# Kernel tuning notes

Hardware: AMD Instinct MI355X
Metric: run time of the kernel (lower is better)

## Reference

```python
import jax, jax.numpy as jnp
import numpy as np

B, S, D, H = 2, 2048, 1024, 16
DK = D // H

def setup_inputs() -> dict:
    key = jax.random.key(0)
    ks = jax.random.split(key, 10)
    s = 1.0 / np.sqrt(D)
    x = jax.random.normal(ks[0], (B, S, D), dtype=jnp.float32)
    # causal mask [B,1,S,S]: 1 = keep, 0 = masked
    mask = jnp.broadcast_to(jnp.tril(jnp.ones((S, S), dtype=jnp.int32))[None, None], (B, 1, S, S))
    wq = jax.random.uniform(ks[1], (D, D), jnp.float32, -s, s)
    bq = jax.random.uniform(ks[2], (D,), jnp.float32, -s, s)
    wk = jax.random.uniform(ks[3], (D, D), jnp.float32, -s, s)
    bk = jax.random.uniform(ks[4], (D,), jnp.float32, -s, s)
    wv = jax.random.uniform(ks[5], (D, D), jnp.float32, -s, s)
    bv = jax.random.uniform(ks[6], (D,), jnp.float32, -s, s)
    wo = jax.random.uniform(ks[7], (D, D), jnp.float32, -s, s)
    bo = jax.random.uniform(ks[8], (D,), jnp.float32, -s, s)
    return {"x": x, "mask": mask, "wq": wq, "bq": bq, "wk": wk, "bk": bk,
            "wv": wv, "bv": bv, "wo": wo, "bo": bo}

def reference(x, mask, wq, bq, wk, bk, wv, bv, wo, bo):
    # projections; torch Linear: y = x @ W^T + b
    def proj(w, b):
        return (jnp.einsum('bsd,ed->bse', x, w) + b).reshape(B, S, H, DK).transpose(0, 2, 1, 3)
    q = proj(wq, bq)  # [B,H,S,DK]
    k = proj(wk, bk)
    v = proj(wv, bv)
    scores = jnp.einsum('bhsd,bhtd->bhst', q, k) / np.sqrt(DK)  # [B,H,S,S]
    scores = jnp.where(mask == 0, jnp.float32(-1e9), scores)
    attn = jax.nn.softmax(scores, axis=-1)
    # dropout in eval mode -> identity
    out = jnp.einsum('bhst,bhtd->bhsd', attn, v)  # [B,H,S,DK]
    out = out.transpose(0, 2, 1, 3).reshape(B, S, D)
    return jnp.einsum('bsd,ed->bse', out, wo) + bo
```

## Files before the change

kernel.cpp:

```cpp
#include <hip/hip_runtime.h>
#include <hip/hip_bf16.h>

#define BB 2
#define SS 2048
#define DD 1024
#define HH 16
#define DK 64
#define MM (BB*SS)

typedef __attribute__((ext_vector_type(8))) short bf16x8;
typedef __attribute__((ext_vector_type(4))) float f32x4;

__device__ inline ushort f2bf(float f) {
  __hip_bfloat16 h = __float2bfloat16(f);
  return *reinterpret_cast<ushort*>(&h);
}

__device__ __forceinline__ float exp2_hw(float x) {
  float r; asm("v_exp_f32 %0, %1" : "=v"(r) : "v"(x)); return r;
}

__device__ __forceinline__ void gl_lds16(const ushort* g, ushort* l) {
  __builtin_amdgcn_global_load_lds((const __attribute__((address_space(1))) void*)g,
                                   (__attribute__((address_space(3))) void*)l, 16, 0, 0);
}

__global__ void cvt_f32_bf16(const float* __restrict__ src, ushort* __restrict__ dst, int n4) {
  int i = blockIdx.x * blockDim.x + threadIdx.x;
  int stride = gridDim.x * blockDim.x;
  for (int idx = i; idx < n4; idx += stride) {
    float4 v = reinterpret_cast<const float4*>(src)[idx];
    ushort4 o;
    o.x = f2bf(v.x); o.y = f2bf(v.y); o.z = f2bf(v.z); o.w = f2bf(v.w);
    reinterpret_cast<ushort4*>(dst)[idx] = o;
  }
}

__global__ void cvt3_f32_bf16(const float* __restrict__ s0, const float* __restrict__ s1,
                              const float* __restrict__ s2, ushort* __restrict__ dst) {
  const int n4seg = DD * DD / 4;
  int i = blockIdx.x * blockDim.x + threadIdx.x;
  int stride = gridDim.x * blockDim.x;
  for (int idx = i; idx < 3 * n4seg; idx += stride) {
    int seg = idx / n4seg;
    int off = idx - seg * n4seg;
    const float* s = (seg == 0) ? s0 : (seg == 1) ? s1 : s2;
    float4 v = reinterpret_cast<const float4*>(s)[off];
    ushort4 o;
    o.x = f2bf(v.x); o.y = f2bf(v.y); o.z = f2bf(v.z); o.w = f2bf(v.w);
    reinterpret_cast<ushort4*>(dst)[idx] = o;
  }
}

__global__ __launch_bounds__(256, 3) void gemm_qkv(const ushort* __restrict__ A,
                                                   const ushort* __restrict__ Wqkv,
                                                   const float* __restrict__ bq,
                                                   const float* __restrict__ bk,
                                                   const float* __restrict__ bv,
                                                   ushort* __restrict__ Qo,
                                                   ushort* __restrict__ Ko,
                                                   ushort* __restrict__ Vo,
                                                   float qscale) {
  constexpr int K = 1024;
  __shared__ __align__(16) ushort lA[128 * 64];
  __shared__ __align__(16) ushort lB[128 * 64];
  const int t = threadIdx.x;
  const int w = t >> 6, lane = t & 63;
  const int flat = blockIdx.x + 24 * blockIdx.y;
  const int xcd = flat & 7, idx = flat >> 3;
  const int m0 = ((xcd << 2) + (idx & 3)) * 128;
  const int n0 = (idx >> 2) * 128;
  const int wm = (w >> 1) * 64, wn = (w & 1) * 64;
  const int c = lane & 15, g = lane >> 4;

  f32x4 acc[4][4];
  #pragma unroll
  for (int i = 0; i < 4; i++)
    #pragma unroll
    for (int j = 0; j < 4; j++) acc[i][j] = f32x4{0.f, 0.f, 0.f, 0.f};

  auto stage = [&](int ks) {
    const int k0 = ks * 64;
    #pragma unroll
    for (int i = 0; i < 4; i++) {
      int ch = w * 256 + i * 64 + lane;
      int row = ch >> 3;
      int cs = (ch & 7) ^ (row & 7);
      gl_lds16(&A[(size_t)(m0 + row) * K + k0 + cs * 8], &lA[(w * 256 + i * 64) * 8]);
      gl_lds16(&Wqkv[(size_t)(n0 + row) * K + k0 + cs * 8], &lB[(w * 256 + i * 64) * 8]);
    }
  };

  for (int ks = 0; ks < 16; ks++) {
    stage(ks);
    __syncthreads();
    #pragma unroll
    for (int kk2 = 0; kk2 < 2; kk2++) {
      bf16x8 af[4], bfr[4];
      #pragma unroll
      for (int mi = 0; mi < 4; mi++) {
        int row = wm + mi * 16 + c;
        af[mi] = *reinterpret_cast<const bf16x8*>(&lA[row * 64 + (((kk2 * 4 + g) ^ (c & 7)) * 8)]);
      }
      #pragma unroll
      for (int ni = 0; ni < 4; ni++) {
        int row = wn + ni * 16 + c;
        bfr[ni] = *reinterpret_cast<const bf16x8*>(&lB[row * 64 + (((kk2 * 4 + g) ^ (c & 7)) * 8)]);
      }
      #pragma unroll
      for (int mi = 0; mi < 4; mi++)
        #pragma unroll
        for (int ni = 0; ni < 4; ni++)
          acc[mi][ni] = __builtin_amdgcn_mfma_f32_16x16x32_bf16(af[mi], bfr[ni], acc[mi][ni], 0, 0, 0);
    }
    __syncthreads();
  }

  const int seg = n0 >> 10;
  const float* bp = (seg == 0) ? bq : (seg == 1) ? bk : bv;
  ushort* op = (seg == 0) ? Qo : Ko;
  const float sc = (seg == 0) ? qscale : 1.0f;
  #pragma unroll
  for (int mi = 0; mi < 4; mi++) {
    #pragma unroll
    for (int ni = 0; ni < 4; ni++) {
      int colq = (n0 + wn + ni * 16 + c) & 1023;
      float bvv = bp[colq];
      int h = colq >> 6, dk = colq & 63;
      #pragma unroll
      for (int j = 0; j < 4; j++) {
        int row = m0 + wm + mi * 16 + g * 4 + j;
        int b = row >> 11, s = row & 2047;
        float val = (acc[mi][ni][j] + bvv) * sc;
        if (seg == 2) {
          Vo[(((b * HH + h) * DK + dk) << 11) + s] = f2bf(val);
        } else {
          op[(((b * HH + h) * SS + s) << 6) + dk] = f2bf(val);
        }
      }
    }
  }
}

__global__ __launch_bounds__(256, 2) void gemm_out(const ushort* __restrict__ A,
                                                   const ushort* __restrict__ W,
                                                   const float* __restrict__ bias,
                                                   float* __restrict__ out) {
  constexpr int K = 1024;
  __shared__ __align__(16) ushort lA[2][64 * 64];
  __shared__ __align__(16) ushort lB[2][128 * 64];
  const int t = threadIdx.x;
  const int w = t >> 6, lane = t & 63;
  const int flat = blockIdx.x + 8 * blockIdx.y;
  const int swz = (flat & 7) * 64 + (flat >> 3);
  const int m0 = (swz >> 3) * 64, n0 = (swz & 7) * 128;
  const int wm = (w >> 1) * 32, wn = (w & 1) * 64;
  const int c = lane & 15, g = lane >> 4;

  f32x4 acc[2][4];
  #pragma unroll
  for (int i = 0; i < 2; i++)
    #pragma unroll
    for (int j = 0; j < 4; j++) acc[i][j] = f32x4{0.f, 0.f, 0.f, 0.f};

  auto stage = [&](int ks, int buf) {
    const int k0 = ks * 64;
    #pragma unroll
    for (int i = 0; i < 2; i++) {
      int ch = i * 256 + t;
      int row = ch >> 3;
      int cs = (ch & 7) ^ (row & 7);
      gl_lds16(&A[(size_t)(m0 + row) * K + k0 + cs * 8], &lA[buf][(i * 256 + w * 64) * 8]);
    }
    #pragma unroll
    for (int i = 0; i < 4; i++) {
      int ch = i * 256 + t;
      int row = ch >> 3;
      int cs = (ch & 7) ^ (row & 7);
      gl_lds16(&W[(size_t)(n0 + row) * K + k0 + cs * 8], &lB[buf][(i * 256 + w * 64) * 8]);
    }
  };

  stage(0, 0);
  __syncthreads();
  int cur = 0;
  for (int ks = 0; ks < 16; ks++) {
    if (ks + 1 < 16) stage(ks + 1, cur ^ 1);
    #pragma unroll
    for (int kk2 = 0; kk2 < 2; kk2++) {
      bf16x8 af[2], bfr[4];
      #pragma unroll
      for (int mi = 0; mi < 2; mi++) {
        int row = wm + mi * 16 + c;
        af[mi] = *reinterpret_cast<const bf16x8*>(&lA[cur][row * 64 + (((kk2 * 4 + g) ^ (c & 7)) * 8)]);
      }
      #pragma unroll
      for (int ni = 0; ni < 4; ni++) {
        int row = wn + ni * 16 + c;
        bfr[ni] = *reinterpret_cast<const bf16x8*>(&lB[cur][row * 64 + (((kk2 * 4 + g) ^ (c & 7)) * 8)]);
      }
      #pragma unroll
      for (int mi = 0; mi < 2; mi++)
        #pragma unroll
        for (int ni = 0; ni < 4; ni++)
          acc[mi][ni] = __builtin_amdgcn_mfma_f32_16x16x32_bf16(af[mi], bfr[ni], acc[mi][ni], 0, 0, 0);
    }
    __syncthreads();
    cur ^= 1;
  }

  #pragma unroll
  for (int mi = 0; mi < 2; mi++) {
    #pragma unroll
    for (int ni = 0; ni < 4; ni++) {
      int colb = n0 + wn + ni * 16 + c;
      float bv = bias[colb];
      #pragma unroll
      for (int j = 0; j < 4; j++) {
        int row = m0 + wm + mi * 16 + g * 4 + j;
        out[(row << 10) + colb] = acc[mi][ni][j] + bv;
      }
    }
  }
}

__global__ __launch_bounds__(256, 2) void attn_fwd(const ushort* __restrict__ Q,
                                                   const ushort* __restrict__ Kk,
                                                   const ushort* __restrict__ Vt,
                                                   ushort* __restrict__ O) {
  __shared__ __align__(16) ushort ldsK[2][64 * 64];
  __shared__ __align__(16) ushort ldsV[2][64 * 64];
  __shared__ __align__(16) ushort lds_p[4][16 * 72];
  const int t0 = threadIdx.x;
  const int w = t0 >> 6;
  const int lane = t0 & 63;
  const int c = lane & 15, g = lane >> 4;
  const int flat = blockIdx.x + 16 * blockIdx.y;
  const int swz = (flat & 7) * 64 + (flat >> 3);
  const int bx = swz & 15;
  const int bh = swz >> 4;
  const int a = bx * 4 + w;
  const int rb0 = a * 16;
  const int rb1 = 2032 - a * 16;
  const int itB = (2111 - 16 * a) >> 6;
  const int itMax = (2111 - 64 * bx) >> 6;

  const ushort* qbase = Q + (size_t)bh * SS * DK;
  const ushort* kbase = Kk + (size_t)bh * SS * DK;
  const ushort* vbase = Vt + (size_t)bh * DK * SS;

  bf16x8 onesf;
  #pragma unroll
  for (int i = 0; i < 8; i++) onesf[i] = (short)0x3F80;

  bf16x8 qf[2][2];
  qf[0][0] = *reinterpret_cast<const bf16x8*>(&qbase[(rb0 + c) * DK + g * 8]);
  qf[0][1] = *reinterpret_cast<const bf16x8*>(&qbase[(rb0 + c) * DK + 32 + g * 8]);
  qf[1][0] = *reinterpret_cast<const bf16x8*>(&qbase[(rb1 + c) * DK + g * 8]);
  qf[1][1] = *reinterpret_cast<const bf16x8*>(&qbase[(rb1 + c) * DK + 32 + g * 8]);

  f32x4 oacc[2][4], lacc[2];
  #pragma unroll
  for (int f = 0; f < 2; f++) {
    #pragma unroll
    for (int i = 0; i < 4; i++) oacc[f][i] = f32x4{0.f, 0.f, 0.f, 0.f};
    lacc[f] = f32x4{0.f, 0.f, 0.f, 0.f};
  }

  auto stage = [&](int tt, int buf) {
    const int kv = tt * 64;
    #pragma unroll
    for (int i = 0; i < 2; i++) {
      int ch = w * 128 + i * 64 + lane;
      int row = ch >> 3;
      int cs = (ch & 7) ^ (row & 7);
      gl_lds16(&kbase[(kv + row) * DK + cs * 8], &ldsK[buf][(w * 128 + i * 64) * 8]);
      gl_lds16(&vbase[row * SS + kv + cs * 8], &ldsV[buf][(w * 128 + i * 64) * 8]);
    }
  };

  stage(0, 0);
  __syncthreads();
  int cur = 0;

  for (int t = 0; t < itMax; ++t) {
    const int kv = t * 64;
    if (t + 1 < itMax) stage(t + 1, cur ^ 1);
    const bool actB = t < itB;
    const bool actA = kv < rb0 + 16;
    if (actA || actB) {
      bf16x8 kf[8];
      #pragma unroll
      for (int i = 0; i < 8; i++) {
        int tt = i >> 1, kk2 = i & 1;
        kf[i] = *reinterpret_cast<const bf16x8*>(
            &ldsK[cur][(tt * 16 + c) * 64 + (((kk2 * 4 + g) ^ (c & 7)) * 8)]);
      }
      f32x4 s[2][4];
      __builtin_amdgcn_s_setprio(1);
      if (actB) {
        #pragma unroll
        for (int tt = 0; tt < 4; tt++) {
          f32x4 z = {0.f, 0.f, 0.f, 0.f};
          z = __builtin_amdgcn_mfma_f32_16x16x32_bf16(qf[1][0], kf[tt * 2], z, 0, 0, 0);
          s[1][tt] = __builtin_amdgcn_mfma_f32_16x16x32_bf16(qf[1][1], kf[tt * 2 + 1], z, 0, 0, 0);
        }
      }
      if (actA) {
        #pragma unroll
        for (int tt = 0; tt < 4; tt++) {
          f32x4 z = {0.f, 0.f, 0.f, 0.f};
          z = __builtin_amdgcn_mfma_f32_16x16x32_bf16(qf[0][0], kf[tt * 2], z, 0, 0, 0);
          s[0][tt] = __builtin_amdgcn_mfma_f32_16x16x32_bf16(qf[0][1], kf[tt * 2 + 1], z, 0, 0, 0);
        }
      }
      __builtin_amdgcn_s_setprio(0);

      bf16x8 vf[8];
      #pragma unroll
      for (int i = 0; i < 8; i++) {
        int dt = i >> 1, kk2 = i & 1;
        vf[i] = *reinterpret_cast<const bf16x8*>(
            &ldsV[cur][(dt * 16 + c) * 64 + (((kk2 * 4 + g) ^ (c & 7)) * 8)]);
      }

      #pragma unroll
      for (int f = 0; f < 2; f++) {
        const bool act = (f == 0) ? actA : actB;
        if (act) {
          const int rbf = (f == 0) ? rb0 : rb1;
          ushort* pb = &lds_p[w][0];
          const bool edge = (kv + 63 > rbf);
          #pragma unroll
          for (int tt = 0; tt < 4; tt++) {
            int kj = kv + tt * 16 + c;
            #pragma unroll
            for (int j = 0; j < 4; j++) {
              float p = exp2_hw(s[f][tt][j]);
              if (edge && kj > rbf + g * 4 + j) p = 0.f;
              pb[(g * 4 + j) * 72 + tt * 16 + c] = f2bf(p);
            }
          }
          __builtin_amdgcn_s_setprio(1);
          #pragma unroll
          for (int kk2 = 0; kk2 < 2; kk2++) {
            bf16x8 pa = *reinterpret_cast<const bf16x8*>(&pb[c * 72 + kk2 * 32 + g * 8]);
            #pragma unroll
            for (int dt = 0; dt < 4; dt++)
              oacc[f][dt] = __builtin_amdgcn_mfma_f32_16x16x32_bf16(pa, vf[dt * 2 + kk2], oacc[f][dt], 0, 0, 0);
            lacc[f] = __builtin_amdgcn_mfma_f32_16x16x32_bf16(pa, onesf, lacc[f], 0, 0, 0);
          }
          __builtin_amdgcn_s_setprio(0);
        }
      }
    }
    __syncthreads();
    cur ^= 1;
  }

  const int b = bh >> 4, h = bh & 15;
  #pragma unroll
  for (int f = 0; f < 2; f++) {
    const int rbf = (f == 0) ? rb0 : rb1;
    #pragma unroll
    for (int j = 0; j < 4; j++) {
      float linv = 1.0f / lacc[f][j];
      int row = rbf + g * 4 + j;
      #pragma unroll
      for (int dt = 0; dt < 4; dt++) {
        float val = oacc[f][dt][j] * linv;
        O[((size_t)(b * SS + row) << 10) + h * DK + dt * 16 + c] = f2bf(val);
      }
    }
  }
}

extern "C" void kernel_launch(void* const* d_in, const int* in_sizes, int n_in,
                              void* d_out, int out_size, void* d_ws, size_t ws_size,
                              hipStream_t stream) {
  const float* x  = (const float*)d_in[0];
  const float* wq = (const float*)d_in[2];
  const float* bq = (const float*)d_in[3];
  const float* wk = (const float*)d_in[4];
  const float* bk = (const float*)d_in[5];
  const float* wv = (const float*)d_in[6];
  const float* bv = (const float*)d_in[7];
  const float* wo = (const float*)d_in[8];
  const float* bo = (const float*)d_in[9];

  ushort* ws = (ushort*)d_ws;
  ushort* xb   = ws;
  ushort* wqkv = xb + (size_t)MM * DD;
  ushort* qw   = wqkv + (size_t)3 * DD * DD;
  ushort* kw   = qw + (size_t)MM * DD;
  ushort* vw   = kw + (size_t)MM * DD;
  ushort* aw   = xb;

  const float qscale = 0.18033688011112043f;

  cvt_f32_bf16<<<2048, 256, 0, stream>>>(x, xb, MM * DD / 4);
  cvt3_f32_bf16<<<1536, 256, 0, stream>>>(wq, wk, wv, wqkv);

  gemm_qkv<<<dim3(24, 32), 256, 0, stream>>>(xb, wqkv, bq, bk, bv, qw, kw, vw, qscale);

  cvt_f32_bf16<<<512, 256, 0, stream>>>(wo, wqkv, DD * DD / 4);

  attn_fwd<<<dim3(16, BB * HH), 256, 0, stream>>>(qw, kw, vw, aw);

  gemm_out<<<dim3(8, 64), 256, 0, stream>>>(aw, wqkv, bo, (float*)d_out);
}
```

Baseline: 113.5 us.

## Fuse weight conversions, shrink out-proj tiles, and stage two KV tiles per attention step

Converts all four weight matrices in a single kernel when the workspace is large enough, which removes one launch between the QKV GEMM and attention. The output GEMM moves to 64x64 tiles with single-buffered LDS and a higher occupancy target, launched on a 16x64 grid with an XCD-aware block mapping. The attention kernel now loads two 64-wide KV tiles per double-buffered stage, halving the number of barriers per key span. The trade-offs are the loss of prefetch overlap in the output GEMM and doubled LDS use in attention, which may lower attention occupancy.

```diff
diff --git a/kernel.cpp b/kernel.cpp
--- a/kernel.cpp
+++ b/kernel.cpp
@@ -45,6 +45,23 @@
     int seg = idx / n4seg;
     int off = idx - seg * n4seg;
     const float* s = (seg == 0) ? s0 : (seg == 1) ? s1 : s2;
+    float4 v = reinterpret_cast<const float4*>(s)[off];
+    ushort4 o;
+    o.x = f2bf(v.x); o.y = f2bf(v.y); o.z = f2bf(v.z); o.w = f2bf(v.w);
+    reinterpret_cast<ushort4*>(dst)[idx] = o;
+  }
+}
+
+__global__ void cvt4_f32_bf16(const float* __restrict__ s0, const float* __restrict__ s1,
+                              const float* __restrict__ s2, const float* __restrict__ s3,
+                              ushort* __restrict__ dst) {
+  const int n4seg = DD * DD / 4;
+  int i = blockIdx.x * blockDim.x + threadIdx.x;
+  int stride = gridDim.x * blockDim.x;
+  for (int idx = i; idx < 4 * n4seg; idx += stride) {
+    int seg = idx / n4seg;
+    int off = idx - seg * n4seg;
+    const float* s = (seg == 0) ? s0 : (seg == 1) ? s1 : (seg == 2) ? s2 : s3;
     float4 v = reinterpret_cast<const float4*>(s)[off];
     ushort4 o;
     o.x = f2bf(v.x); o.y = f2bf(v.y); o.z = f2bf(v.z); o.w = f2bf(v.w);
@@ -142,77 +159,69 @@
   }
 }
 
-__global__ __launch_bounds__(256, 2) void gemm_out(const ushort* __restrict__ A,
+__global__ __launch_bounds__(256, 4) void gemm_out(const ushort* __restrict__ A,
                                                    const ushort* __restrict__ W,
                                                    const float* __restrict__ bias,
                                                    float* __restrict__ out) {
   constexpr int K = 1024;
-  __shared__ __align__(16) ushort lA[2][64 * 64];
-  __shared__ __align__(16) ushort lB[2][128 * 64];
+  __shared__ __align__(16) ushort lA[64 * 64];
+  __shared__ __align__(16) ushort lB[64 * 64];
   const int t = threadIdx.x;
   const int w = t >> 6, lane = t & 63;
-  const int flat = blockIdx.x + 8 * blockIdx.y;
-  const int swz = (flat & 7) * 64 + (flat >> 3);
-  const int m0 = (swz >> 3) * 64, n0 = (swz & 7) * 128;
-  const int wm = (w >> 1) * 32, wn = (w & 1) * 64;
+  const int flat = blockIdx.x + 16 * blockIdx.y;
+  const int xcd = flat & 7, idx = flat >> 3;
+  const int m0 = ((xcd << 3) + (idx & 7)) * 64;
+  const int n0 = (idx >> 3) * 64;
+  const int wm = (w >> 1) * 32, wn = (w & 1) * 32;
   const int c = lane & 15, g = lane >> 4;
 
-  f32x4 acc[2][4];
+  f32x4 acc[2][2];
   #pragma unroll
   for (int i = 0; i < 2; i++)
     #pragma unroll
-    for (int j = 0; j < 4; j++) acc[i][j] = f32x4{0.f, 0.f, 0.f, 0.f};
-
-  auto stage = [&](int ks, int buf) {
+    for (int j = 0; j < 2; j++) acc[i][j] = f32x4{0.f, 0.f, 0.f, 0.f};
+
+  auto stage = [&](int ks) {
     const int k0 = ks * 64;
     #pragma unroll
     for (int i = 0; i < 2; i++) {
       int ch = i * 256 + t;
       int row = ch >> 3;
       int cs = (ch & 7) ^ (row & 7);
-      gl_lds16(&A[(size_t)(m0 + row) * K + k0 + cs * 8], &lA[buf][(i * 256 + w * 64) * 8]);
-    }
-    #pragma unroll
-    for (int i = 0; i < 4; i++) {
-      int ch = i * 256 + t;
-      int row = ch >> 3;
-      int cs = (ch & 7) ^ (row & 7);
-      gl_lds16(&W[(size_t)(n0 + row) * K + k0 + cs * 8], &lB[buf][(i * 256 + w * 64) * 8]);
+      gl_lds16(&A[(size_t)(m0 + row) * K + k0 + cs * 8], &lA[(i * 256 + w * 64) * 8]);
+      gl_lds16(&W[(size_t)(n0 + row) * K + k0 + cs * 8], &lB[(i * 256 + w * 64) * 8]);
     }
   };
 
-  stage(0, 0);
-  __syncthreads();
-  int cur = 0;
   for (int ks = 0; ks < 16; ks++) {
-    if (ks + 1 < 16) stage(ks + 1, cur ^ 1);
+    stage(ks);
+    __syncthreads();
     #pragma unroll
     for (int kk2 = 0; kk2 < 2; kk2++) {
-      bf16x8 af[2], bfr[4];
+      bf16x8 af[2], bfr[2];
       #pragma unroll
       for (int mi = 0; mi < 2; mi++) {
         int row = wm + mi * 16 + c;
-        af[mi] = *reinterpret_cast<const bf16x8*>(&lA[cur][row * 64 + (((kk2 * 4 + g) ^ (c & 7)) * 8)]);
-      }
-      #pragma unroll
-      for (int ni = 0; ni < 4; ni++) {
+        af[mi] = *reinterpret_cast<const bf16x8*>(&lA[row * 64 + (((kk2 * 4 + g) ^ (c & 7)) * 8)]);
+      }
+      #pragma unroll
+      for (int ni = 0; ni < 2; ni++) {
         int row = wn + ni * 16 + c;
-        bfr[ni] = *reinterpret_cast<const bf16x8*>(&lB[cur][row * 64 + (((kk2 * 4 + g) ^ (c & 7)) * 8)]);
+        bfr[ni] = *reinterpret_cast<const bf16x8*>(&lB[row * 64 + (((kk2 * 4 + g) ^ (c & 7)) * 8)]);
       }
       #pragma unroll
       for (int mi = 0; mi < 2; mi++)
         #pragma unroll
-        for (int ni = 0; ni < 4; ni++)
+        for (int ni = 0; ni < 2; ni++)
           acc[mi][ni] = __builtin_amdgcn_mfma_f32_16x16x32_bf16(af[mi], bfr[ni], acc[mi][ni], 0, 0, 0);
     }
     __syncthreads();
-    cur ^= 1;
   }
 
   #pragma unroll
   for (int mi = 0; mi < 2; mi++) {
     #pragma unroll
-    for (int ni = 0; ni < 4; ni++) {
+    for (int ni = 0; ni < 2; ni++) {
       int colb = n0 + wn + ni * 16 + c;
       float bv = bias[colb];
       #pragma unroll
@@ -228,8 +237,8 @@
                                                    const ushort* __restrict__ Kk,
                                                    const ushort* __restrict__ Vt,
                                                    ushort* __restrict__ O) {
-  __shared__ __align__(16) ushort ldsK[2][64 * 64];
-  __shared__ __align__(16) ushort ldsV[2][64 * 64];
+  __shared__ __align__(16) ushort ldsK[2][2][64 * 64];
+  __shared__ __align__(16) ushort ldsV[2][2][64 * 64];
   __shared__ __align__(16) ushort lds_p[4][16 * 72];
   const int t0 = threadIdx.x;
   const int w = t0 >> 6;
@@ -244,6 +253,7 @@
   const int rb1 = 2032 - a * 16;
   const int itB = (2111 - 16 * a) >> 6;
   const int itMax = (2111 - 64 * bx) >> 6;
+  const int nS = (itMax + 1) >> 1;
 
   const ushort* qbase = Q + (size_t)bh * SS * DK;
   const ushort* kbase = Kk + (size_t)bh * SS * DK;
@@ -267,15 +277,19 @@
     lacc[f] = f32x4{0.f, 0.f, 0.f, 0.f};
   }
 
-  auto stage = [&](int tt, int buf) {
-    const int kv = tt * 64;
-    #pragma unroll
-    for (int i = 0; i < 2; i++) {
-      int ch = w * 128 + i * 64 + lane;
-      int row = ch >> 3;
-      int cs = (ch & 7) ^ (row & 7);
-      gl_lds16(&kbase[(kv + row) * DK + cs * 8], &ldsK[buf][(w * 128 + i * 64) * 8]);
-      gl_lds16(&vbase[row * SS + kv + cs * 8], &ldsV[buf][(w * 128 + i * 64) * 8]);
+  auto stage = [&](int st, int buf) {
+    #pragma unroll
+    for (int half = 0; half < 2; half++) {
+      int tt = 2 * st + half; if (tt > 31) tt = 31;
+      const int kv = tt * 64;
+      #pragma unroll
+      for (int i = 0; i < 2; i++) {
+        int ch = w * 128 + i * 64 + lane;
+        int row = ch >> 3;
+        int cs = (ch & 7) ^ (row & 7);
+        gl_lds16(&kbase[(kv + row) * DK + cs * 8], &ldsK[buf][half][(w * 128 + i * 64) * 8]);
+        gl_lds16(&vbase[row * SS + kv + cs * 8], &ldsV[buf][half][(w * 128 + i * 64) * 8]);
+      }
     }
   };
 
@@ -283,74 +297,79 @@
   __syncthreads();
   int cur = 0;
 
-  for (int t = 0; t < itMax; ++t) {
-    const int kv = t * 64;
-    if (t + 1 < itMax) stage(t + 1, cur ^ 1);
-    const bool actB = t < itB;
-    const bool actA = kv < rb0 + 16;
-    if (actA || actB) {
-      bf16x8 kf[8];
-      #pragma unroll
-      for (int i = 0; i < 8; i++) {
-        int tt = i >> 1, kk2 = i & 1;
-        kf[i] = *reinterpret_cast<const bf16x8*>(
-            &ldsK[cur][(tt * 16 + c) * 64 + (((kk2 * 4 + g) ^ (c & 7)) * 8)]);
-      }
-      f32x4 s[2][4];
-      __builtin_amdgcn_s_setprio(1);
-      if (actB) {
+  for (int st = 0; st < nS; ++st) {
+    if (st + 1 < nS) stage(st + 1, cur ^ 1);
+    #pragma unroll
+    for (int half = 0; half < 2; half++) {
+      const int t = 2 * st + half;
+      const int kv = t * 64;
+      const bool run = t < itMax;
+      const bool actB = run && (t < itB);
+      const bool actA = run && (kv < rb0 + 16);
+      if (actA || actB) {
+        bf16x8 kf[8];
         #pragma unroll
-        for (int tt = 0; tt < 4; tt++) {
-          f32x4 z = {0.f, 0.f, 0.f, 0.f};
-          z = __builtin_amdgcn_mfma_f32_16x16x32_bf16(qf[1][0], kf[tt * 2], z, 0, 0, 0);
-          s[1][tt] = __builtin_amdgcn_mfma_f32_16x16x32_bf16(qf[1][1], kf[tt * 2 + 1], z, 0, 0, 0);
-        }
-      }
-      if (actA) {
-        #pragma unroll
-        for (int tt = 0; tt < 4; tt++) {
-          f32x4 z = {0.f, 0.f, 0.f, 0.f};
-          z = __builtin_amdgcn_mfma_f32_16x16x32_bf16(qf[0][0], kf[tt * 2], z, 0, 0, 0);
-          s[0][tt] = __builtin_amdgcn_mfma_f32_16x16x32_bf16(qf[0][1], kf[tt * 2 + 1], z, 0, 0, 0);
-        }
-      }
-      __builtin_amdgcn_s_setprio(0);
-
-      bf16x8 vf[8];
-      #pragma unroll
-      for (int i = 0; i < 8; i++) {
-        int dt = i >> 1, kk2 = i & 1;
-        vf[i] = *reinterpret_cast<const bf16x8*>(
-            &ldsV[cur][(dt * 16 + c) * 64 + (((kk2 * 4 + g) ^ (c & 7)) * 8)]);
-      }
-
-      #pragma unroll
-      for (int f = 0; f < 2; f++) {
-        const bool act = (f == 0) ? actA : actB;
-        if (act) {
-          const int rbf = (f == 0) ? rb0 : rb1;
-          ushort* pb = &lds_p[w][0];
-          const bool edge = (kv + 63 > rbf);
+        for (int i = 0; i < 8; i++) {
+          int tt = i >> 1, kk2 = i & 1;
+          kf[i] = *reinterpret_cast<const bf16x8*>(
+              &ldsK[cur][half][(tt * 16 + c) * 64 + (((kk2 * 4 + g) ^ (c & 7)) * 8)]);
+        }
+        f32x4 s[2][4];
+        __builtin_amdgcn_s_setprio(1);
+        if (actB) {
           #pragma unroll
           for (int tt = 0; tt < 4; tt++) {
-            int kj = kv + tt * 16 + c;
+            f32x4 z = {0.f, 0.f, 0.f, 0.f};
+            z = __builtin_amdgcn_mfma_f32_16x16x32_bf16(qf[1][0], kf[tt * 2], z, 0, 0, 0);
+            s[1][tt] = __builtin_amdgcn_mfma_f32_16x16x32_bf16(qf[1][1], kf[tt * 2 + 1], z, 0, 0, 0);
+          }
+        }
+        if (actA) {
+          #pragma unroll
+          for (int tt = 0; tt < 4; tt++) {
+            f32x4 z = {0.f, 0.f, 0.f, 0.f};
+            z = __builtin_amdgcn_mfma_f32_16x16x32_bf16(qf[0][0], kf[tt * 2], z, 0, 0, 0);
+            s[0][tt] = __builtin_amdgcn_mfma_f32_16x16x32_bf16(qf[0][1], kf[tt * 2 + 1], z, 0, 0, 0);
+          }
+        }
+        __builtin_amdgcn_s_setprio(0);
+
+        bf16x8 vf[8];
+        #pragma unroll
+        for (int i = 0; i < 8; i++) {
+          int dt = i >> 1, kk2 = i & 1;
+          vf[i] = *reinterpret_cast<const bf16x8*>(
+              &ldsV[cur][half][(dt * 16 + c) * 64 + (((kk2 * 4 + g) ^ (c & 7)) * 8)]);
+        }
+
+        #pragma unroll
+        for (int f = 0; f < 2; f++) {
+          const bool act = (f == 0) ? actA : actB;
+          if (act) {
+            const int rbf = (f == 0) ? rb0 : rb1;
+            ushort* pb = &lds_p[w][0];
+            const bool edge = (kv + 63 > rbf);
             #pragma unroll
-            for (int j = 0; j < 4; j++) {
-              float p = exp2_hw(s[f][tt][j]);
-              if (edge && kj > rbf + g * 4 + j) p = 0.f;
-              pb[(g * 4 + j) * 72 + tt * 16 + c] = f2bf(p);
+            for (int tt = 0; tt < 4; tt++) {
+              int kj = kv + tt * 16 + c;
+              #pragma unroll
+              for (int j = 0; j < 4; j++) {
+                float p = exp2_hw(s[f][tt][j]);
+                if (edge && kj > rbf + g * 4 + j) p = 0.f;
+                pb[(g * 4 + j) * 72 + tt * 16 + c] = f2bf(p);
+              }
             }
+            __builtin_amdgcn_s_setprio(1);
+            #pragma unroll
+            for (int kk2 = 0; kk2 < 2; kk2++) {
+              bf16x8 pa = *reinterpret_cast<const bf16x8*>(&pb[c * 72 + kk2 * 32 + g * 8]);
+              #pragma unroll
+              for (int dt = 0; dt < 4; dt++)
+                oacc[f][dt] = __builtin_amdgcn_mfma_f32_16x16x32_bf16(pa, vf[dt * 2 + kk2], oacc[f][dt], 0, 0, 0);
+              lacc[f] = __builtin_amdgcn_mfma_f32_16x16x32_bf16(pa, onesf, lacc[f], 0, 0, 0);
+            }
+            __builtin_amdgcn_s_setprio(0);
           }
-          __builtin_amdgcn_s_setprio(1);
-          #pragma unroll
-          for (int kk2 = 0; kk2 < 2; kk2++) {
-            bf16x8 pa = *reinterpret_cast<const bf16x8*>(&pb[c * 72 + kk2 * 32 + g * 8]);
-            #pragma unroll
-            for (int dt = 0; dt < 4; dt++)
-              oacc[f][dt] = __builtin_amdgcn_mfma_f32_16x16x32_bf16(pa, vf[dt * 2 + kk2], oacc[f][dt], 0, 0, 0);
-            lacc[f] = __builtin_amdgcn_mfma_f32_16x16x32_bf16(pa, onesf, lacc[f], 0, 0, 0);
-          }
-          __builtin_amdgcn_s_setprio(0);
         }
       }
     }
@@ -391,21 +410,29 @@
   ushort* ws = (ushort*)d_ws;
   ushort* xb   = ws;
   ushort* wqkv = xb + (size_t)MM * DD;
-  ushort* qw   = wqkv + (size_t)3 * DD * DD;
-  ushort* kw   = qw + (size_t)MM * DD;
-  ushort* vw   = kw + (size_t)MM * DD;
-  ushort* aw   = xb;
 
   const float qscale = 0.18033688011112043f;
+  const size_t needA = (size_t)(4 + 4 + 4 * 4) * DD * DD * sizeof(ushort);
 
   cvt_f32_bf16<<<2048, 256, 0, stream>>>(x, xb, MM * DD / 4);
-  cvt3_f32_bf16<<<1536, 256, 0, stream>>>(wq, wk, wv, wqkv);
-
-  gemm_qkv<<<dim3(24, 32), 256, 0, stream>>>(xb, wqkv, bq, bk, bv, qw, kw, vw, qscale);
-
-  cvt_f32_bf16<<<512, 256, 0, stream>>>(wo, wqkv, DD * DD / 4);
-
-  attn_fwd<<<dim3(16, BB * HH), 256, 0, stream>>>(qw, kw, vw, aw);
-
-  gemm_out<<<dim3(8, 64), 256, 0, stream>>>(aw, wqkv, bo, (float*)d_out);
-}
+
+  if (ws_size >= needA) {
+    ushort* wob = wqkv + (size_t)3 * DD * DD;
+    ushort* qw  = wob + (size_t)DD * DD;
+    ushort* kw  = qw + (size_t)MM * DD;
+    ushort* vw  = kw + (size_t)MM * DD;
+    cvt4_f32_bf16<<<2048, 256, 0, stream>>>(wq, wk, wv, wo, wqkv);
+    gemm_qkv<<<dim3(24, 32), 256, 0, stream>>>(xb, wqkv, bq, bk, bv, qw, kw, vw, qscale);
+    attn_fwd<<<dim3(16, BB * HH), 256, 0, stream>>>(qw, kw, vw, xb);
+    gemm_out<<<dim3(16, 64), 256, 0, stream>>>(xb, wob, bo, (float*)d_out);
+  } else {
+    ushort* qw = wqkv + (size_t)3 * DD * DD;
+    ushort* kw = qw + (size_t)MM * DD;
+    ushort* vw = kw + (size_t)MM * DD;
+    cvt3_f32_bf16<<<1536, 256, 0, stream>>>(wq, wk, wv, wqkv);
+    gemm_qkv<<<dim3(24, 32), 256, 0, stream>>>(xb, wqkv, bq, bk, bv, qw, kw, vw, qscale);
+    cvt_f32_bf16<<<512, 256, 0, stream>>>(wo, wqkv, DD * DD / 4);
+    attn_fwd<<<dim3(16, BB * HH), 256, 0, stream>>>(qw, kw, vw, xb);
+    gemm_out<<<dim3(16, 64), 256, 0, stream>>>(xb, wqkv, bo, (float*)d_out);
+  }
+}
```

New measurement: 103.3 us. 1.1x faster.
